# Optimization experiments

Measured on AMD Instinct MI355X. Metric: run time of the kernel, lower is better.

Reference implementation:

```python
import jax, jax.numpy as jnp
import numpy as np
import math

DIM = 1024
MAX_SEQ_LEN = 8192

def setup_inputs() -> dict:
    key = jax.random.key(0)
    k1, k2, k3, k4 = jax.random.split(key, 4)
    x = jax.random.normal(k1, (4, 4096, DIM), dtype=jnp.float32)
    base_phases = jax.random.normal(k2, (MAX_SEQ_LEN, DIM), dtype=jnp.float32) * math.pi
    # nn.Linear(dim, dim): weight [out, in], bias [out]
    bound = 1.0 / math.sqrt(DIM)
    W = jax.random.uniform(k3, (DIM, DIM), dtype=jnp.float32, minval=-bound, maxval=bound)
    b = jax.random.uniform(k4, (DIM,), dtype=jnp.float32, minval=-bound, maxval=bound)
    return {"x": x, "base_phases": base_phases, "W": W, "b": b}

def reference(x, base_phases, W, b):
    B, L, D = x.shape
    phases = base_phases[:L][None, :, :]          # [1, L, D]
    value = jnp.einsum('bld,ed->ble', x, W) + b   # Linear: x @ W.T + b
    cos_p = jnp.cos(phases)
    sin_p = jnp.sin(phases)
    mem_real = jnp.cumsum(value * cos_p, axis=1)
    mem_imag = jnp.cumsum(value * sin_p, axis=1)
    retrieved = mem_real * cos_p + mem_imag * sin_p
    positions = jnp.arange(1, L + 1, dtype=jnp.float32)
    norm = jnp.sqrt(positions)[None, :, None]     # [1, L, 1]
    return retrieved / norm
```

## Files before the change

kernel.cpp:

```cpp
#include <hip/hip_runtime.h>
#include <hip/hip_bf16.h>

#define DIM 1024
#define SEQ 4096
#define NB 4
#define MROWS (NB * SEQ)
#define NC 64
#define CL (SEQ / NC)

#define BM 256
#define BN 256
#define BK 32
#define NT (DIM / BK)
#define TILE_LDS 32768
#define GEMM_LDS (4 * TILE_LDS)

typedef __attribute__((ext_vector_type(8))) short bf16x8;
typedef __attribute__((ext_vector_type(4))) float f32x4;

static __device__ __forceinline__ unsigned short f2bf(float f) {
    union { float f; unsigned u; } v; v.f = f;
    unsigned r = v.u + 0x7FFF + ((v.u >> 16) & 1);
    return (unsigned short)(r >> 16);
}

static __device__ __forceinline__ float bf2f(unsigned short h) {
    union { unsigned u; float f; } v; v.u = ((unsigned)h) << 16;
    return v.f;
}

static __device__ __forceinline__ void gload_lds16(const void* g, void* l) {
    __builtin_amdgcn_global_load_lds((const __attribute__((address_space(1))) void*)g,
                                     (__attribute__((address_space(3))) void*)l, 16, 0, 0);
}

__global__ void convert_kernel(const float* __restrict__ x, const float* __restrict__ W,
                               unsigned short* __restrict__ xb, unsigned short* __restrict__ wb) {
    const long long NX4 = (long long)MROWS * DIM / 4;
    const long long NW4 = (long long)DIM * DIM / 4;
    long long t = (long long)blockIdx.x * blockDim.x + threadIdx.x;
    if (t < NX4) {
        float4 v = ((const float4*)x)[t];
        ushort4 o;
        o.x = f2bf(v.x); o.y = f2bf(v.y); o.z = f2bf(v.z); o.w = f2bf(v.w);
        ((ushort4*)xb)[t] = o;
    } else if (t < NX4 + NW4) {
        long long u = t - NX4;
        float4 v = ((const float4*)W)[u];
        ushort4 o;
        o.x = f2bf(v.x); o.y = f2bf(v.y); o.z = f2bf(v.z); o.w = f2bf(v.w);
        ((ushort4*)wb)[u] = o;
    }
}

static __device__ __forceinline__ void stage_A(const unsigned short* __restrict__ A, char* smem,
                                               int q, int m0, int ks, int w, int lane) {
    const int c16 = (lane & 3) ^ ((lane >> 3) & 3);
#pragma unroll
    for (int r = 0; r < 2; ++r) {
        int row = r * 128 + w * 16 + (lane >> 2);
        const unsigned short* g = A + (size_t)(m0 + row) * DIM + ks + c16 * 8;
        char* l = smem + q * TILE_LDS + (r * 128 + w * 16) * 64 + lane * 16;
        gload_lds16(g, l);
    }
}

static __device__ __forceinline__ void stage_B(const unsigned short* __restrict__ Bm, char* smem,
                                               int q, int n0, int ks, int w, int lane) {
    const int c16 = (lane & 3) ^ ((lane >> 3) & 3);
#pragma unroll
    for (int r = 0; r < 2; ++r) {
        int row = r * 128 + w * 16 + (lane >> 2);
        const unsigned short* g = Bm + (size_t)(n0 + row) * DIM + ks + c16 * 8;
        char* l = smem + q * TILE_LDS + 16384 + (r * 128 + w * 16) * 64 + lane * 16;
        gload_lds16(g, l);
    }
}

__global__ __launch_bounds__(512, 2) void gemm_kernel(const unsigned short* __restrict__ A,
                                                      const unsigned short* __restrict__ Bm,
                                                      const float* __restrict__ bias,
                                                      unsigned short* __restrict__ V) {
    extern __shared__ char smem[];
    const int tid  = threadIdx.x;
    const int lane = tid & 63;
    const int w    = tid >> 6;
    const int wm   = w >> 2;
    const int wn   = w & 3;
    const int wr   = wm * 128;
    const int wc   = wn * 64;
    const int rl   = lane & 15;
    const int rh   = lane >> 4;
    const int swz  = (rh ^ ((rl >> 1) & 3)) * 16;
    const int m0   = blockIdx.x * BM;
    const int n0   = blockIdx.y * BN;

    f32x4 acc[8][4];
#pragma unroll
    for (int m = 0; m < 8; ++m)
#pragma unroll
        for (int n = 0; n < 4; ++n)
            acc[m][n] = (f32x4){0.f, 0.f, 0.f, 0.f};

    float bv[4];
#pragma unroll
    for (int nf = 0; nf < 4; ++nf)
        bv[nf] = bias[n0 + wc + nf * 16 + rl];

#pragma unroll
    for (int s = 0; s < 3; ++s) {
        stage_A(A, smem, s, m0, s * BK, w, lane);
        stage_B(Bm, smem, s, n0, s * BK, w, lane);
    }
    asm volatile("s_waitcnt vmcnt(8)" ::: "memory");
    __builtin_amdgcn_s_barrier();

#pragma unroll 4
    for (int t = 0; t < NT; ++t) {
        const int q  = t & 3;
        const int qn = (t + 3) & 3;
        const int ksn = ((t + 3) & (NT - 1)) * BK;
        char* base = smem + q * TILE_LDS;

        bf16x8 bfr[4];
#pragma unroll
        for (int nf = 0; nf < 4; ++nf)
            bfr[nf] = *(const bf16x8*)(base + 16384 + (wc + nf * 16 + rl) * 64 + swz);
        bf16x8 af[4];
#pragma unroll
        for (int mf = 0; mf < 4; ++mf)
            af[mf] = *(const bf16x8*)(base + (wr + mf * 16 + rl) * 64 + swz);
        stage_A(A, smem, qn, m0, ksn, w, lane);
        __builtin_amdgcn_sched_barrier(0);
        __builtin_amdgcn_s_barrier();
        asm volatile("s_waitcnt lgkmcnt(0)" ::: "memory");
        __builtin_amdgcn_sched_barrier(0);
        __builtin_amdgcn_s_setprio(1);
#pragma unroll
        for (int mf = 0; mf < 4; ++mf)
#pragma unroll
            for (int nf = 0; nf < 4; ++nf)
                acc[mf][nf] = __builtin_amdgcn_mfma_f32_16x16x32_bf16(af[mf], bfr[nf], acc[mf][nf], 0, 0, 0);
        __builtin_amdgcn_s_setprio(0);
        __builtin_amdgcn_sched_barrier(0);
        __builtin_amdgcn_s_barrier();

#pragma unroll
        for (int mf = 0; mf < 4; ++mf)
            af[mf] = *(const bf16x8*)(base + (wr + (mf + 4) * 16 + rl) * 64 + swz);
        stage_B(Bm, smem, qn, n0, ksn, w, lane);
        asm volatile("s_waitcnt vmcnt(8)" ::: "memory");
        __builtin_amdgcn_sched_barrier(0);
        __builtin_amdgcn_s_barrier();
        asm volatile("s_waitcnt lgkmcnt(0)" ::: "memory");
        __builtin_amdgcn_sched_barrier(0);
        __builtin_amdgcn_s_setprio(1);
#pragma unroll
        for (int mf = 0; mf < 4; ++mf)
#pragma unroll
            for (int nf = 0; nf < 4; ++nf)
                acc[mf + 4][nf] = __builtin_amdgcn_mfma_f32_16x16x32_bf16(af[mf], bfr[nf], acc[mf + 4][nf], 0, 0, 0);
        __builtin_amdgcn_s_setprio(0);
        __builtin_amdgcn_sched_barrier(0);
        __builtin_amdgcn_s_barrier();
    }

#pragma unroll
    for (int mf = 0; mf < 8; ++mf) {
#pragma unroll
        for (int nf = 0; nf < 4; ++nf) {
            int gcol = n0 + wc + nf * 16 + rl;
#pragma unroll
            for (int j = 0; j < 4; ++j) {
                int grow = m0 + wr + mf * 16 + rh * 4 + j;
                V[(size_t)grow * DIM + gcol] = f2bf(acc[mf][nf][j] + bv[nf]);
            }
        }
    }
}

__global__ void passA_kernel(const unsigned short* __restrict__ val, const float* __restrict__ ph,
                             float* __restrict__ pr, float* __restrict__ pi) {
    int t  = blockIdx.x * 256 + threadIdx.x;
    int c  = blockIdx.y;
    int bb = blockIdx.z;
    const ushort2* v = (const ushort2*)val + ((size_t)bb * SEQ + (size_t)c * CL) * (DIM / 2) + t;
    const float2*  p = (const float2*)ph + (size_t)c * CL * (DIM / 2) + t;
    float sr0 = 0.f, si0 = 0.f, sr1 = 0.f, si1 = 0.f;
    for (int l = 0; l < CL; ++l) {
        ushort2 vv = v[(size_t)l * (DIM / 2)];
        float2  pp = p[(size_t)l * (DIM / 2)];
        float v0 = bf2f(vv.x), v1 = bf2f(vv.y);
        float s0, c0, s1, c1;
        __sincosf(pp.x, &s0, &c0);
        __sincosf(pp.y, &s1, &c1);
        sr0 += v0 * c0; si0 += v0 * s0;
        sr1 += v1 * c1; si1 += v1 * s1;
    }
    size_t idx = ((size_t)bb * NC + c) * DIM + 2 * t;
    pr[idx] = sr0; pr[idx + 1] = sr1;
    pi[idx] = si0; pi[idx + 1] = si1;
}

__global__ void passB_kernel(float* __restrict__ pr, float* __restrict__ pi) {
    int t = blockIdx.x * 256 + threadIdx.x;
    int bb = t >> 10;
    int e  = t & 1023;
    float r = 0.f, im = 0.f;
    for (int c = 0; c < NC; ++c) {
        size_t idx = ((size_t)bb * NC + c) * DIM + e;
        float tr = pr[idx], ti = pi[idx];
        pr[idx] = r; pi[idx] = im;
        r += tr; im += ti;
    }
}

__global__ void passC_kernel(const unsigned short* __restrict__ val, const float* __restrict__ ph,
                             const float* __restrict__ pr, const float* __restrict__ pi,
                             float* __restrict__ out) {
    int t  = blockIdx.x * 256 + threadIdx.x;
    int c  = blockIdx.y;
    int bb = blockIdx.z;
    size_t base = ((size_t)bb * SEQ + (size_t)c * CL) * (DIM / 2) + t;
    const ushort2* v = (const ushort2*)val + base;
    const float2*  p = (const float2*)ph + (size_t)c * CL * (DIM / 2) + t;
    float2* o = (float2*)out + base;
    size_t pidx = ((size_t)bb * NC + c) * DIM + 2 * t;
    float ar0 = pr[pidx], ar1 = pr[pidx + 1];
    float ai0 = pi[pidx], ai1 = pi[pidx + 1];
    const int l0 = c * CL;
    for (int l = 0; l < CL; ++l) {
        ushort2 vv = v[(size_t)l * (DIM / 2)];
        float2  pp = p[(size_t)l * (DIM / 2)];
        float v0 = bf2f(vv.x), v1 = bf2f(vv.y);
        float s0, c0, s1, c1;
        __sincosf(pp.x, &s0, &c0);
        __sincosf(pp.y, &s1, &c1);
        ar0 += v0 * c0; ai0 += v0 * s0;
        ar1 += v1 * c1; ai1 += v1 * s1;
        float rn = rsqrtf((float)(l0 + l + 1));
        float2 ov;
        ov.x = (ar0 * c0 + ai0 * s0) * rn;
        ov.y = (ar1 * c1 + ai1 * s1) * rn;
        o[(size_t)l * (DIM / 2)] = ov;
    }
}

extern "C" void kernel_launch(void* const* d_in, const int* in_sizes, int n_in,
                              void* d_out, int out_size, void* d_ws, size_t ws_size,
                              hipStream_t stream) {
    const float* x  = (const float*)d_in[0];
    const float* ph = (const float*)d_in[1];
    const float* W  = (const float*)d_in[2];
    const float* b  = (const float*)d_in[3];
    float* out = (float*)d_out;

    unsigned short* xb = (unsigned short*)d_out;
    unsigned short* wb = xb + (size_t)MROWS * DIM;

    unsigned short* vb = (unsigned short*)d_ws;
    float* pr = (float*)(vb + (size_t)MROWS * DIM);
    float* pi = pr + (size_t)NB * NC * DIM;

    (void)hipFuncSetAttribute((const void*)gemm_kernel,
                              hipFuncAttributeMaxDynamicSharedMemorySize, GEMM_LDS);

    {
        long long total4 = (long long)MROWS * DIM / 4 + (long long)DIM * DIM / 4;
        int blocks = (int)((total4 + 255) / 256);
        convert_kernel<<<blocks, 256, 0, stream>>>(x, W, xb, wb);
    }
    {
        dim3 grid(MROWS / BM, DIM / BN);
        gemm_kernel<<<grid, 512, GEMM_LDS, stream>>>(xb, wb, b, vb);
    }
    {
        dim3 grid(DIM / 512, NC, NB);
        passA_kernel<<<grid, 256, 0, stream>>>(vb, ph, pr, pi);
    }
    passB_kernel<<<16, 256, 0, stream>>>(pr, pi);
    {
        dim3 grid(DIM / 512, NC, NB);
        passC_kernel<<<grid, 256, 0, stream>>>(vb, ph, pr, pi, out);
    }
}
```

Baseline: 93.76 us.

## Fuse chunked scan passes into single-pass decoupled look-back kernel; trim GEMM barriers

Replaces the three-kernel chunked scan (per-chunk aggregates, serial prefix over chunks, final pass) with one kernel. Each block publishes its chunk aggregate and inclusive prefix through flags, and later blocks do a decoupled look-back instead of waiting for a separate prefix kernel. This removes two kernel launches and the serial prefix pass. It also cuts the GEMM main loop down to one wait and barrier per k-step instead of four, and drops the explicit LDS waits. That risks races on the LDS buffers, since stages are overwritten while other waves may still be reading them. The look-back assumes earlier blocks are scheduled first, which holds here because the grid is only 256 blocks.

After: 264.8 us. 2.82x slower.

```diff
diff --git a/kernel.cpp b/kernel.cpp
--- a/kernel.cpp
+++ b/kernel.cpp
@@ -112,14 +112,14 @@
         stage_A(A, smem, s, m0, s * BK, w, lane);
         stage_B(Bm, smem, s, n0, s * BK, w, lane);
     }
-    asm volatile("s_waitcnt vmcnt(8)" ::: "memory");
-    __builtin_amdgcn_s_barrier();
 
 #pragma unroll 4
     for (int t = 0; t < NT; ++t) {
         const int q  = t & 3;
         const int qn = (t + 3) & 3;
         const int ksn = ((t + 3) & (NT - 1)) * BK;
+        asm volatile("s_waitcnt vmcnt(8)" ::: "memory");
+        __builtin_amdgcn_s_barrier();
         char* base = smem + q * TILE_LDS;
 
         bf16x8 bfr[4];
@@ -131,10 +131,6 @@
         for (int mf = 0; mf < 4; ++mf)
             af[mf] = *(const bf16x8*)(base + (wr + mf * 16 + rl) * 64 + swz);
         stage_A(A, smem, qn, m0, ksn, w, lane);
-        __builtin_amdgcn_sched_barrier(0);
-        __builtin_amdgcn_s_barrier();
-        asm volatile("s_waitcnt lgkmcnt(0)" ::: "memory");
-        __builtin_amdgcn_sched_barrier(0);
         __builtin_amdgcn_s_setprio(1);
 #pragma unroll
         for (int mf = 0; mf < 4; ++mf)
@@ -142,18 +138,11 @@
             for (int nf = 0; nf < 4; ++nf)
                 acc[mf][nf] = __builtin_amdgcn_mfma_f32_16x16x32_bf16(af[mf], bfr[nf], acc[mf][nf], 0, 0, 0);
         __builtin_amdgcn_s_setprio(0);
-        __builtin_amdgcn_sched_barrier(0);
-        __builtin_amdgcn_s_barrier();
 
 #pragma unroll
         for (int mf = 0; mf < 4; ++mf)
             af[mf] = *(const bf16x8*)(base + (wr + (mf + 4) * 16 + rl) * 64 + swz);
         stage_B(Bm, smem, qn, n0, ksn, w, lane);
-        asm volatile("s_waitcnt vmcnt(8)" ::: "memory");
-        __builtin_amdgcn_sched_barrier(0);
-        __builtin_amdgcn_s_barrier();
-        asm volatile("s_waitcnt lgkmcnt(0)" ::: "memory");
-        __builtin_amdgcn_sched_barrier(0);
         __builtin_amdgcn_s_setprio(1);
 #pragma unroll
         for (int mf = 0; mf < 4; ++mf)
@@ -161,8 +150,6 @@
             for (int nf = 0; nf < 4; ++nf)
                 acc[mf + 4][nf] = __builtin_amdgcn_mfma_f32_16x16x32_bf16(af[mf], bfr[nf], acc[mf + 4][nf], 0, 0, 0);
         __builtin_amdgcn_s_setprio(0);
-        __builtin_amdgcn_sched_barrier(0);
-        __builtin_amdgcn_s_barrier();
     }
 
 #pragma unroll
@@ -179,70 +166,93 @@
     }
 }
 
-__global__ void passA_kernel(const unsigned short* __restrict__ val, const float* __restrict__ ph,
-                             float* __restrict__ pr, float* __restrict__ pi) {
-    int t  = blockIdx.x * 256 + threadIdx.x;
-    int c  = blockIdx.y;
-    int bb = blockIdx.z;
-    const ushort2* v = (const ushort2*)val + ((size_t)bb * SEQ + (size_t)c * CL) * (DIM / 2) + t;
-    const float2*  p = (const float2*)ph + (size_t)c * CL * (DIM / 2) + t;
-    float sr0 = 0.f, si0 = 0.f, sr1 = 0.f, si1 = 0.f;
+__global__ __launch_bounds__(256) void scan_kernel(const unsigned short* __restrict__ vb,
+                                                   const float* __restrict__ ph,
+                                                   float* __restrict__ aggR, float* __restrict__ aggI,
+                                                   float* __restrict__ preR, float* __restrict__ preI,
+                                                   int* __restrict__ flags,
+                                                   float* __restrict__ out) {
+    const int tid = threadIdx.x;
+    const int c   = blockIdx.x & (NC - 1);
+    const int b   = blockIdx.x >> 6;
+    const int l0  = c * CL;
+    const int e0  = tid * 4;
+    const size_t vbase = ((size_t)b * SEQ + l0) * DIM + e0;
+    const size_t pbase = (size_t)l0 * DIM + e0;
+
+    float ar[4] = {0.f, 0.f, 0.f, 0.f}, ai[4] = {0.f, 0.f, 0.f, 0.f};
     for (int l = 0; l < CL; ++l) {
-        ushort2 vv = v[(size_t)l * (DIM / 2)];
-        float2  pp = p[(size_t)l * (DIM / 2)];
-        float v0 = bf2f(vv.x), v1 = bf2f(vv.y);
-        float s0, c0, s1, c1;
-        __sincosf(pp.x, &s0, &c0);
-        __sincosf(pp.y, &s1, &c1);
-        sr0 += v0 * c0; si0 += v0 * s0;
-        sr1 += v1 * c1; si1 += v1 * s1;
-    }
-    size_t idx = ((size_t)bb * NC + c) * DIM + 2 * t;
-    pr[idx] = sr0; pr[idx + 1] = sr1;
-    pi[idx] = si0; pi[idx + 1] = si1;
-}
-
-__global__ void passB_kernel(float* __restrict__ pr, float* __restrict__ pi) {
-    int t = blockIdx.x * 256 + threadIdx.x;
-    int bb = t >> 10;
-    int e  = t & 1023;
-    float r = 0.f, im = 0.f;
-    for (int c = 0; c < NC; ++c) {
-        size_t idx = ((size_t)bb * NC + c) * DIM + e;
-        float tr = pr[idx], ti = pi[idx];
-        pr[idx] = r; pi[idx] = im;
-        r += tr; im += ti;
-    }
-}
-
-__global__ void passC_kernel(const unsigned short* __restrict__ val, const float* __restrict__ ph,
-                             const float* __restrict__ pr, const float* __restrict__ pi,
-                             float* __restrict__ out) {
-    int t  = blockIdx.x * 256 + threadIdx.x;
-    int c  = blockIdx.y;
-    int bb = blockIdx.z;
-    size_t base = ((size_t)bb * SEQ + (size_t)c * CL) * (DIM / 2) + t;
-    const ushort2* v = (const ushort2*)val + base;
-    const float2*  p = (const float2*)ph + (size_t)c * CL * (DIM / 2) + t;
-    float2* o = (float2*)out + base;
-    size_t pidx = ((size_t)bb * NC + c) * DIM + 2 * t;
-    float ar0 = pr[pidx], ar1 = pr[pidx + 1];
-    float ai0 = pi[pidx], ai1 = pi[pidx + 1];
-    const int l0 = c * CL;
+        ushort4 vv = *(const ushort4*)(vb + vbase + (size_t)l * DIM);
+        float4  pp = *(const float4*)(ph + pbase + (size_t)l * DIM);
+        float v[4] = {bf2f(vv.x), bf2f(vv.y), bf2f(vv.z), bf2f(vv.w)};
+        float p[4] = {pp.x, pp.y, pp.z, pp.w};
+#pragma unroll
+        for (int k = 0; k < 4; ++k) {
+            float s, cn;
+            __sincosf(p[k], &s, &cn);
+            ar[k] += v[k] * cn;
+            ai[k] += v[k] * s;
+        }
+    }
+
+    const size_t idx  = ((size_t)b * NC + c) * DIM + e0;
+    const int    fidx = b * NC + c;
+    if (c > 0) {
+        *(float4*)(aggR + idx) = (float4){ar[0], ar[1], ar[2], ar[3]};
+        *(float4*)(aggI + idx) = (float4){ai[0], ai[1], ai[2], ai[3]};
+        __syncthreads();
+        __threadfence();
+        if (tid == 0)
+            __hip_atomic_store(flags + fidx, 1, __ATOMIC_RELEASE, __HIP_MEMORY_SCOPE_AGENT);
+    }
+
+    float pr[4] = {0.f, 0.f, 0.f, 0.f}, pi[4] = {0.f, 0.f, 0.f, 0.f};
+    if (c > 0) {
+        int cc = c - 1;
+        for (;;) {
+            int st;
+            do {
+                st = __hip_atomic_load(flags + b * NC + cc, __ATOMIC_ACQUIRE, __HIP_MEMORY_SCOPE_AGENT);
+            } while (st == 0);
+            size_t cidx = ((size_t)b * NC + cc) * DIM + e0;
+            if (st == 2) {
+                float4 r  = *(const float4*)(preR + cidx);
+                float4 im = *(const float4*)(preI + cidx);
+                pr[0] += r.x;  pr[1] += r.y;  pr[2] += r.z;  pr[3] += r.w;
+                pi[0] += im.x; pi[1] += im.y; pi[2] += im.z; pi[3] += im.w;
+                break;
+            }
+            float4 r  = *(const float4*)(aggR + cidx);
+            float4 im = *(const float4*)(aggI + cidx);
+            pr[0] += r.x;  pr[1] += r.y;  pr[2] += r.z;  pr[3] += r.w;
+            pi[0] += im.x; pi[1] += im.y; pi[2] += im.z; pi[3] += im.w;
+            --cc;
+        }
+    }
+
+    *(float4*)(preR + idx) = (float4){pr[0] + ar[0], pr[1] + ar[1], pr[2] + ar[2], pr[3] + ar[3]};
+    *(float4*)(preI + idx) = (float4){pi[0] + ai[0], pi[1] + ai[1], pi[2] + ai[2], pi[3] + ai[3]};
+    __syncthreads();
+    __threadfence();
+    if (tid == 0)
+        __hip_atomic_store(flags + fidx, 2, __ATOMIC_RELEASE, __HIP_MEMORY_SCOPE_AGENT);
+
     for (int l = 0; l < CL; ++l) {
-        ushort2 vv = v[(size_t)l * (DIM / 2)];
-        float2  pp = p[(size_t)l * (DIM / 2)];
-        float v0 = bf2f(vv.x), v1 = bf2f(vv.y);
-        float s0, c0, s1, c1;
-        __sincosf(pp.x, &s0, &c0);
-        __sincosf(pp.y, &s1, &c1);
-        ar0 += v0 * c0; ai0 += v0 * s0;
-        ar1 += v1 * c1; ai1 += v1 * s1;
+        ushort4 vv = *(const ushort4*)(vb + vbase + (size_t)l * DIM);
+        float4  pp = *(const float4*)(ph + pbase + (size_t)l * DIM);
+        float v[4] = {bf2f(vv.x), bf2f(vv.y), bf2f(vv.z), bf2f(vv.w)};
+        float p[4] = {pp.x, pp.y, pp.z, pp.w};
         float rn = rsqrtf((float)(l0 + l + 1));
-        float2 ov;
-        ov.x = (ar0 * c0 + ai0 * s0) * rn;
-        ov.y = (ar1 * c1 + ai1 * s1) * rn;
-        o[(size_t)l * (DIM / 2)] = ov;
+        float o[4];
+#pragma unroll
+        for (int k = 0; k < 4; ++k) {
+            float s, cn;
+            __sincosf(p[k], &s, &cn);
+            pr[k] += v[k] * cn;
+            pi[k] += v[k] * s;
+            o[k] = (pr[k] * cn + pi[k] * s) * rn;
+        }
+        *(float4*)(out + vbase + (size_t)l * DIM) = (float4){o[0], o[1], o[2], o[3]};
     }
 }
 
@@ -259,11 +269,16 @@
     unsigned short* wb = xb + (size_t)MROWS * DIM;
 
     unsigned short* vb = (unsigned short*)d_ws;
-    float* pr = (float*)(vb + (size_t)MROWS * DIM);
-    float* pi = pr + (size_t)NB * NC * DIM;
+    float* aggR = (float*)(vb + (size_t)MROWS * DIM);
+    float* aggI = aggR + (size_t)NB * NC * DIM;
+    float* preR = aggI + (size_t)NB * NC * DIM;
+    float* preI = preR + (size_t)NB * NC * DIM;
+    int*   flags = (int*)(preI + (size_t)NB * NC * DIM);
 
     (void)hipFuncSetAttribute((const void*)gemm_kernel,
                               hipFuncAttributeMaxDynamicSharedMemorySize, GEMM_LDS);
+
+    hipMemsetAsync(flags, 0, NB * NC * sizeof(int), stream);
 
     {
         long long total4 = (long long)MROWS * DIM / 4 + (long long)DIM * DIM / 4;
@@ -274,13 +289,5 @@
         dim3 grid(MROWS / BM, DIM / BN);
         gemm_kernel<<<grid, 512, GEMM_LDS, stream>>>(xb, wb, b, vb);
     }
-    {
-        dim3 grid(DIM / 512, NC, NB);
-        passA_kernel<<<grid, 256, 0, stream>>>(vb, ph, pr, pi);
-    }
-    passB_kernel<<<16, 256, 0, stream>>>(pr, pi);
-    {
-        dim3 grid(DIM / 512, NC, NB);
-        passC_kernel<<<grid, 256, 0, stream>>>(vb, ph, pr, pi, out);
-    }
-}
+    scan_kernel<<<NB * NC, 256, 0, stream>>>(vb, ph, aggR, aggI, preR, preI, flags, out);
+}
```

## Fuse fp32-to-bf16 conversion of x into GEMM A-tile staging

Applied to the files above, without the earlier changes.

Drops the separate pass that converted x to bf16. The GEMM now loads fp32 rows of x into registers, packs them to bf16 and writes them to LDS itself, and only W is still converted in a small standalone kernel. The main loop is reorganised around one barrier per K step, with B prefetched two stages ahead and A held in registers one stage ahead. This removes a 64MB read plus 32MB write round trip through a separate kernel, but doubles the GEMM's global read bytes for A, adds VGPR pressure, and replaces the async LDS loads for A with synchronous register stores.

New measurement: 90.33 us. 3.7% less time.

```diff
diff --git a/kernel.cpp b/kernel.cpp
--- a/kernel.cpp
+++ b/kernel.cpp
@@ -29,40 +29,30 @@
     return v.f;
 }
 
+static __device__ __forceinline__ unsigned int bfpair(float a, float b) {
+    unsigned ua = __float_as_uint(a), ub = __float_as_uint(b);
+    unsigned ra = (ua + 0x7FFF + ((ua >> 16) & 1)) >> 16;
+    unsigned rb = (ub + 0x7FFF + ((ub >> 16) & 1)) & 0xFFFF0000u;
+    return ra | rb;
+}
+static __device__ __forceinline__ uint4 packbf8(float4 lo, float4 hi) {
+    uint4 r;
+    r.x = bfpair(lo.x, lo.y); r.y = bfpair(lo.z, lo.w);
+    r.z = bfpair(hi.x, hi.y); r.w = bfpair(hi.z, hi.w);
+    return r;
+}
+
 static __device__ __forceinline__ void gload_lds16(const void* g, void* l) {
     __builtin_amdgcn_global_load_lds((const __attribute__((address_space(1))) void*)g,
                                      (__attribute__((address_space(3))) void*)l, 16, 0, 0);
 }
 
-__global__ void convert_kernel(const float* __restrict__ x, const float* __restrict__ W,
-                               unsigned short* __restrict__ xb, unsigned short* __restrict__ wb) {
-    const long long NX4 = (long long)MROWS * DIM / 4;
-    const long long NW4 = (long long)DIM * DIM / 4;
-    long long t = (long long)blockIdx.x * blockDim.x + threadIdx.x;
-    if (t < NX4) {
-        float4 v = ((const float4*)x)[t];
-        ushort4 o;
-        o.x = f2bf(v.x); o.y = f2bf(v.y); o.z = f2bf(v.z); o.w = f2bf(v.w);
-        ((ushort4*)xb)[t] = o;
-    } else if (t < NX4 + NW4) {
-        long long u = t - NX4;
-        float4 v = ((const float4*)W)[u];
-        ushort4 o;
-        o.x = f2bf(v.x); o.y = f2bf(v.y); o.z = f2bf(v.z); o.w = f2bf(v.w);
-        ((ushort4*)wb)[u] = o;
-    }
-}
-
-static __device__ __forceinline__ void stage_A(const unsigned short* __restrict__ A, char* smem,
-                                               int q, int m0, int ks, int w, int lane) {
-    const int c16 = (lane & 3) ^ ((lane >> 3) & 3);
-#pragma unroll
-    for (int r = 0; r < 2; ++r) {
-        int row = r * 128 + w * 16 + (lane >> 2);
-        const unsigned short* g = A + (size_t)(m0 + row) * DIM + ks + c16 * 8;
-        char* l = smem + q * TILE_LDS + (r * 128 + w * 16) * 64 + lane * 16;
-        gload_lds16(g, l);
-    }
+__global__ void convertW_kernel(const float* __restrict__ W, unsigned short* __restrict__ wb) {
+    int t = blockIdx.x * 256 + threadIdx.x;
+    float4 v = ((const float4*)W)[t];
+    ushort4 o;
+    o.x = f2bf(v.x); o.y = f2bf(v.y); o.z = f2bf(v.z); o.w = f2bf(v.w);
+    ((ushort4*)wb)[t] = o;
 }
 
 static __device__ __forceinline__ void stage_B(const unsigned short* __restrict__ Bm, char* smem,
@@ -77,7 +67,7 @@
     }
 }
 
-__global__ __launch_bounds__(512, 2) void gemm_kernel(const unsigned short* __restrict__ A,
+__global__ __launch_bounds__(512, 2) void gemm_kernel(const float* __restrict__ X,
                                                       const unsigned short* __restrict__ Bm,
                                                       const float* __restrict__ bias,
                                                       unsigned short* __restrict__ V) {
@@ -94,6 +84,9 @@
     const int swz  = (rh ^ ((rl >> 1) & 3)) * 16;
     const int m0   = blockIdx.x * BM;
     const int n0   = blockIdx.y * BN;
+    const int c16  = (lane & 3) ^ ((lane >> 3) & 3);
+    const int arow = w * 16 + (lane >> 2);
+    const size_t dstA = (size_t)(w * 16) * 64 + (size_t)lane * 16;
 
     f32x4 acc[8][4];
 #pragma unroll
@@ -107,20 +100,40 @@
     for (int nf = 0; nf < 4; ++nf)
         bv[nf] = bias[n0 + wc + nf * 16 + rl];
 
-#pragma unroll
-    for (int s = 0; s < 3; ++s) {
-        stage_A(A, smem, s, m0, s * BK, w, lane);
-        stage_B(Bm, smem, s, n0, s * BK, w, lane);
-    }
-    asm volatile("s_waitcnt vmcnt(8)" ::: "memory");
+    const float* Xa = X + (size_t)(m0 + arow) * DIM + c16 * 8;
+    const float* Xb = X + (size_t)(m0 + 128 + arow) * DIM + c16 * 8;
+
+    float4 aCl0, aCh0, aCl1, aCh1;
+    float4 aNl0, aNh0, aNl1, aNh1;
+
+    {
+        aCl0 = *(const float4*)(Xa + 0); aCh0 = *(const float4*)(Xa + 4);
+        aCl1 = *(const float4*)(Xb + 0); aCh1 = *(const float4*)(Xb + 4);
+        *(uint4*)(smem + 0 * TILE_LDS + dstA)             = packbf8(aCl0, aCh0);
+        *(uint4*)(smem + 0 * TILE_LDS + 128 * 64 + dstA)  = packbf8(aCl1, aCh1);
+        stage_B(Bm, smem, 0, n0, 0, w, lane);
+        aCl0 = *(const float4*)(Xa + BK); aCh0 = *(const float4*)(Xa + BK + 4);
+        aCl1 = *(const float4*)(Xb + BK); aCh1 = *(const float4*)(Xb + BK + 4);
+        *(uint4*)(smem + 1 * TILE_LDS + dstA)             = packbf8(aCl0, aCh0);
+        *(uint4*)(smem + 1 * TILE_LDS + 128 * 64 + dstA)  = packbf8(aCl1, aCh1);
+        stage_B(Bm, smem, 1, n0, BK, w, lane);
+        aCl0 = *(const float4*)(Xa + 2 * BK); aCh0 = *(const float4*)(Xa + 2 * BK + 4);
+        aCl1 = *(const float4*)(Xb + 2 * BK); aCh1 = *(const float4*)(Xb + 2 * BK + 4);
+    }
+    asm volatile("s_waitcnt lgkmcnt(0)" ::: "memory");
     __builtin_amdgcn_s_barrier();
 
 #pragma unroll 4
     for (int t = 0; t < NT; ++t) {
-        const int q  = t & 3;
-        const int qn = (t + 3) & 3;
-        const int ksn = ((t + 3) & (NT - 1)) * BK;
+        const int q   = t & 3;
+        const int qw  = (t + 2) & 3;
+        const int ksB = ((t + 2) & (NT - 1)) * BK;
+        const int ksA = ((t + 3) & (NT - 1)) * BK;
         char* base = smem + q * TILE_LDS;
+
+        stage_B(Bm, smem, qw, n0, ksB, w, lane);
+        aNl0 = *(const float4*)(Xa + ksA); aNh0 = *(const float4*)(Xa + ksA + 4);
+        aNl1 = *(const float4*)(Xb + ksA); aNh1 = *(const float4*)(Xb + ksA + 4);
 
         bf16x8 bfr[4];
 #pragma unroll
@@ -130,11 +143,6 @@
 #pragma unroll
         for (int mf = 0; mf < 4; ++mf)
             af[mf] = *(const bf16x8*)(base + (wr + mf * 16 + rl) * 64 + swz);
-        stage_A(A, smem, qn, m0, ksn, w, lane);
-        __builtin_amdgcn_sched_barrier(0);
-        __builtin_amdgcn_s_barrier();
-        asm volatile("s_waitcnt lgkmcnt(0)" ::: "memory");
-        __builtin_amdgcn_sched_barrier(0);
         __builtin_amdgcn_s_setprio(1);
 #pragma unroll
         for (int mf = 0; mf < 4; ++mf)
@@ -142,18 +150,13 @@
             for (int nf = 0; nf < 4; ++nf)
                 acc[mf][nf] = __builtin_amdgcn_mfma_f32_16x16x32_bf16(af[mf], bfr[nf], acc[mf][nf], 0, 0, 0);
         __builtin_amdgcn_s_setprio(0);
-        __builtin_amdgcn_sched_barrier(0);
-        __builtin_amdgcn_s_barrier();
+
+        *(uint4*)(smem + qw * TILE_LDS + dstA)            = packbf8(aCl0, aCh0);
+        *(uint4*)(smem + qw * TILE_LDS + 128 * 64 + dstA) = packbf8(aCl1, aCh1);
 
 #pragma unroll
         for (int mf = 0; mf < 4; ++mf)
             af[mf] = *(const bf16x8*)(base + (wr + (mf + 4) * 16 + rl) * 64 + swz);
-        stage_B(Bm, smem, qn, n0, ksn, w, lane);
-        asm volatile("s_waitcnt vmcnt(8)" ::: "memory");
-        __builtin_amdgcn_sched_barrier(0);
-        __builtin_amdgcn_s_barrier();
-        asm volatile("s_waitcnt lgkmcnt(0)" ::: "memory");
-        __builtin_amdgcn_sched_barrier(0);
         __builtin_amdgcn_s_setprio(1);
 #pragma unroll
         for (int mf = 0; mf < 4; ++mf)
@@ -161,6 +164,11 @@
             for (int nf = 0; nf < 4; ++nf)
                 acc[mf + 4][nf] = __builtin_amdgcn_mfma_f32_16x16x32_bf16(af[mf], bfr[nf], acc[mf + 4][nf], 0, 0, 0);
         __builtin_amdgcn_s_setprio(0);
+
+        aCl0 = aNl0; aCh0 = aNh0; aCl1 = aNl1; aCh1 = aNh1;
+
+        asm volatile("s_waitcnt vmcnt(6)" ::: "memory");
+        asm volatile("s_waitcnt lgkmcnt(0)" ::: "memory");
         __builtin_amdgcn_sched_barrier(0);
         __builtin_amdgcn_s_barrier();
     }
@@ -255,24 +263,18 @@
     const float* b  = (const float*)d_in[3];
     float* out = (float*)d_out;
 
-    unsigned short* xb = (unsigned short*)d_out;
-    unsigned short* wb = xb + (size_t)MROWS * DIM;
-
     unsigned short* vb = (unsigned short*)d_ws;
-    float* pr = (float*)(vb + (size_t)MROWS * DIM);
+    unsigned short* wb = vb + (size_t)MROWS * DIM;
+    float* pr = (float*)(wb + (size_t)DIM * DIM);
     float* pi = pr + (size_t)NB * NC * DIM;
 
     (void)hipFuncSetAttribute((const void*)gemm_kernel,
                               hipFuncAttributeMaxDynamicSharedMemorySize, GEMM_LDS);
 
-    {
-        long long total4 = (long long)MROWS * DIM / 4 + (long long)DIM * DIM / 4;
-        int blocks = (int)((total4 + 255) / 256);
-        convert_kernel<<<blocks, 256, 0, stream>>>(x, W, xb, wb);
-    }
+    convertW_kernel<<<DIM * DIM / 4 / 256, 256, 0, stream>>>(W, wb);
     {
         dim3 grid(MROWS / BM, DIM / BN);
-        gemm_kernel<<<grid, 512, GEMM_LDS, stream>>>(xb, wb, b, vb);
+        gemm_kernel<<<grid, 512, GEMM_LDS, stream>>>(x, wb, b, vb);
     }
     {
         dim3 grid(DIM / 512, NC, NB);
```

## Restructure GEMM LDS pipeline into two 64-wide K slots with half-tile staging

Applied to the files above, without the earlier changes.

Replaces the four-slot ring of 32-wide K tiles with two 64 KB slots, each holding a 64-wide K tile split into two 32-wide halves. Loads are issued at half-tile granularity. The main loop becomes a non-unrolled loop of eight phases per iteration, built from a templated do_phase helper. The aim is cleaner address arithmetic and a more regular load/compute interleave, at the cost of a shallower effective prefetch distance and a different wait pattern. The number of K steps and barriers per step stays essentially the same.

Measured after the change: 92.85 us. No clear change (-1.0%).

```diff
diff --git a/kernel.cpp b/kernel.cpp
--- a/kernel.cpp
+++ b/kernel.cpp
@@ -10,10 +10,10 @@
 
 #define BM 256
 #define BN 256
-#define BK 32
-#define NT (DIM / BK)
-#define TILE_LDS 32768
-#define GEMM_LDS (4 * TILE_LDS)
+#define NTILE 16
+#define NITER 8
+#define SLOT_BYTES 65536
+#define GEMM_LDS (2 * SLOT_BYTES)
 
 typedef __attribute__((ext_vector_type(8))) short bf16x8;
 typedef __attribute__((ext_vector_type(4))) float f32x4;
@@ -53,28 +53,46 @@
     }
 }
 
-static __device__ __forceinline__ void stage_A(const unsigned short* __restrict__ A, char* smem,
-                                               int q, int m0, int ks, int w, int lane) {
-    const int c16 = (lane & 3) ^ ((lane >> 3) & 3);
-#pragma unroll
-    for (int r = 0; r < 2; ++r) {
-        int row = r * 128 + w * 16 + (lane >> 2);
-        const unsigned short* g = A + (size_t)(m0 + row) * DIM + ks + c16 * 8;
-        char* l = smem + q * TILE_LDS + (r * 128 + w * 16) * 64 + lane * 16;
-        gload_lds16(g, l);
-    }
-}
-
-static __device__ __forceinline__ void stage_B(const unsigned short* __restrict__ Bm, char* smem,
-                                               int q, int n0, int ks, int w, int lane) {
-    const int c16 = (lane & 3) ^ ((lane >> 3) & 3);
-#pragma unroll
-    for (int r = 0; r < 2; ++r) {
-        int row = r * 128 + w * 16 + (lane >> 2);
-        const unsigned short* g = Bm + (size_t)(n0 + row) * DIM + ks + c16 * 8;
-        char* l = smem + q * TILE_LDS + 16384 + (r * 128 + w * 16) * 64 + lane * 16;
-        gload_lds16(g, l);
-    }
+static __device__ __forceinline__ void stage_ht(const unsigned short* __restrict__ src, char* smem,
+                                                int r0, int tile, int ks, int ab, int tid) {
+    const int sc16 = (tid & 3) ^ ((tid >> 3) & 3);
+    char* dst = smem + (size_t)(tile & 1) * SLOT_BYTES + ab * 32768 + ks * 16384
+              + (tid >> 2) * 64 + (tid & 3) * 16;
+    const unsigned short* g = src + (size_t)(r0 + (tid >> 2)) * DIM
+                            + (tile & (NTILE - 1)) * 64 + ks * 32 + sc16 * 8;
+    gload_lds16(g, dst);
+    gload_lds16(g + (size_t)128 * DIM, dst + 128 * 64);
+}
+
+template<int MFB, bool LOADB, bool VM>
+static __device__ __forceinline__ void do_phase(const char* sbase, int ks,
+    const unsigned short* __restrict__ ssrc, char* smem, int sr0, int stile, int sks, int sab,
+    int tid, int wr, int wc, int rl, int swz, f32x4 acc[8][4], bf16x8 bfr[4])
+{
+    bf16x8 af[4];
+    if (LOADB) {
+#pragma unroll
+        for (int nf = 0; nf < 4; ++nf)
+            bfr[nf] = *(const bf16x8*)(sbase + 32768 + ks * 16384 + (wc + nf * 16 + rl) * 64 + swz);
+    }
+#pragma unroll
+    for (int mf = 0; mf < 4; ++mf)
+        af[mf] = *(const bf16x8*)(sbase + ks * 16384 + (wr + (MFB + mf) * 16 + rl) * 64 + swz);
+    stage_ht(ssrc, smem, sr0, stile, sks, sab, tid);
+    if (VM) asm volatile("s_waitcnt vmcnt(8)" ::: "memory");
+    __builtin_amdgcn_sched_barrier(0);
+    __builtin_amdgcn_s_barrier();
+    asm volatile("s_waitcnt lgkmcnt(0)" ::: "memory");
+    __builtin_amdgcn_sched_barrier(0);
+    __builtin_amdgcn_s_setprio(1);
+#pragma unroll
+    for (int mf = 0; mf < 4; ++mf)
+#pragma unroll
+        for (int nf = 0; nf < 4; ++nf)
+            acc[MFB + mf][nf] = __builtin_amdgcn_mfma_f32_16x16x32_bf16(af[mf], bfr[nf], acc[MFB + mf][nf], 0, 0, 0);
+    __builtin_amdgcn_s_setprio(0);
+    __builtin_amdgcn_sched_barrier(0);
+    __builtin_amdgcn_s_barrier();
 }
 
 __global__ __launch_bounds__(512, 2) void gemm_kernel(const unsigned short* __restrict__ A,
@@ -85,15 +103,15 @@
     const int tid  = threadIdx.x;
     const int lane = tid & 63;
     const int w    = tid >> 6;
-    const int wm   = w >> 2;
-    const int wn   = w & 3;
-    const int wr   = wm * 128;
-    const int wc   = wn * 64;
+    const int wr   = (w >> 2) * 128;
+    const int wc   = (w & 3) * 64;
     const int rl   = lane & 15;
     const int rh   = lane >> 4;
     const int swz  = (rh ^ ((rl >> 1) & 3)) * 16;
     const int m0   = blockIdx.x * BM;
     const int n0   = blockIdx.y * BN;
+    const char* s0 = smem;
+    const char* s1 = smem + SLOT_BYTES;
 
     f32x4 acc[8][4];
 #pragma unroll
@@ -107,62 +125,27 @@
     for (int nf = 0; nf < 4; ++nf)
         bv[nf] = bias[n0 + wc + nf * 16 + rl];
 
-#pragma unroll
-    for (int s = 0; s < 3; ++s) {
-        stage_A(A, smem, s, m0, s * BK, w, lane);
-        stage_B(Bm, smem, s, n0, s * BK, w, lane);
-    }
+    stage_ht(A,  smem, m0, 0, 0, 0, tid);
+    stage_ht(Bm, smem, n0, 0, 0, 1, tid);
+    stage_ht(A,  smem, m0, 0, 1, 0, tid);
+    stage_ht(Bm, smem, n0, 0, 1, 1, tid);
+    stage_ht(A,  smem, m0, 1, 0, 0, tid);
+    stage_ht(Bm, smem, n0, 1, 0, 1, tid);
     asm volatile("s_waitcnt vmcnt(8)" ::: "memory");
     __builtin_amdgcn_s_barrier();
 
-#pragma unroll 4
-    for (int t = 0; t < NT; ++t) {
-        const int q  = t & 3;
-        const int qn = (t + 3) & 3;
-        const int ksn = ((t + 3) & (NT - 1)) * BK;
-        char* base = smem + q * TILE_LDS;
-
-        bf16x8 bfr[4];
-#pragma unroll
-        for (int nf = 0; nf < 4; ++nf)
-            bfr[nf] = *(const bf16x8*)(base + 16384 + (wc + nf * 16 + rl) * 64 + swz);
-        bf16x8 af[4];
-#pragma unroll
-        for (int mf = 0; mf < 4; ++mf)
-            af[mf] = *(const bf16x8*)(base + (wr + mf * 16 + rl) * 64 + swz);
-        stage_A(A, smem, qn, m0, ksn, w, lane);
-        __builtin_amdgcn_sched_barrier(0);
-        __builtin_amdgcn_s_barrier();
-        asm volatile("s_waitcnt lgkmcnt(0)" ::: "memory");
-        __builtin_amdgcn_sched_barrier(0);
-        __builtin_amdgcn_s_setprio(1);
-#pragma unroll
-        for (int mf = 0; mf < 4; ++mf)
-#pragma unroll
-            for (int nf = 0; nf < 4; ++nf)
-                acc[mf][nf] = __builtin_amdgcn_mfma_f32_16x16x32_bf16(af[mf], bfr[nf], acc[mf][nf], 0, 0, 0);
-        __builtin_amdgcn_s_setprio(0);
-        __builtin_amdgcn_sched_barrier(0);
-        __builtin_amdgcn_s_barrier();
-
-#pragma unroll
-        for (int mf = 0; mf < 4; ++mf)
-            af[mf] = *(const bf16x8*)(base + (wr + (mf + 4) * 16 + rl) * 64 + swz);
-        stage_B(Bm, smem, qn, n0, ksn, w, lane);
-        asm volatile("s_waitcnt vmcnt(8)" ::: "memory");
-        __builtin_amdgcn_sched_barrier(0);
-        __builtin_amdgcn_s_barrier();
-        asm volatile("s_waitcnt lgkmcnt(0)" ::: "memory");
-        __builtin_amdgcn_sched_barrier(0);
-        __builtin_amdgcn_s_setprio(1);
-#pragma unroll
-        for (int mf = 0; mf < 4; ++mf)
-#pragma unroll
-            for (int nf = 0; nf < 4; ++nf)
-                acc[mf + 4][nf] = __builtin_amdgcn_mfma_f32_16x16x32_bf16(af[mf], bfr[nf], acc[mf + 4][nf], 0, 0, 0);
-        __builtin_amdgcn_s_setprio(0);
-        __builtin_amdgcn_sched_barrier(0);
-        __builtin_amdgcn_s_barrier();
+    bf16x8 bfr[4];
+#pragma unroll 1
+    for (int i = 0; i < NITER; ++i) {
+        const int t1 = 2 * i + 1, t2 = 2 * i + 2, t3 = 2 * i + 3;
+        do_phase<0, true,  false>(s0, 0, A,  smem, m0, t1, 1, 0, tid, wr, wc, rl, swz, acc, bfr);
+        do_phase<4, false, true >(s0, 0, Bm, smem, n0, t1, 1, 1, tid, wr, wc, rl, swz, acc, bfr);
+        do_phase<0, true,  false>(s0, 1, A,  smem, m0, t2, 0, 0, tid, wr, wc, rl, swz, acc, bfr);
+        do_phase<4, false, true >(s0, 1, Bm, smem, n0, t2, 0, 1, tid, wr, wc, rl, swz, acc, bfr);
+        do_phase<0, true,  false>(s1, 0, A,  smem, m0, t2, 1, 0, tid, wr, wc, rl, swz, acc, bfr);
+        do_phase<4, false, true >(s1, 0, Bm, smem, n0, t2, 1, 1, tid, wr, wc, rl, swz, acc, bfr);
+        do_phase<0, true,  false>(s1, 1, A,  smem, m0, t3, 0, 0, tid, wr, wc, rl, swz, acc, bfr);
+        do_phase<4, false, true >(s1, 1, Bm, smem, n0, t3, 0, 1, tid, wr, wc, rl, swz, acc, bfr);
     }
 
 #pragma unroll
```
